# Kernel tuning notes

Hardware: AMD Instinct MI355X
Metric: run time of the kernel (lower is better)

The kernel has to match this reference:

```python
import jax, jax.numpy as jnp
import numpy as np


def setup_inputs() -> dict:
    key = jax.random.key(0)
    k1, k2, k3, k4, k5, k6 = jax.random.split(key, 6)
    B, N, D, H = 32, 4096, 256, 256
    return {
        "queries": jax.random.normal(k1, (B, N, D), dtype=jnp.float32),
        "keys": jax.random.normal(k2, (B, N, D), dtype=jnp.float32),
        "values": jax.random.normal(k3, (B, N, D), dtype=jnp.float32),
        "Wq": jax.random.normal(k4, (H, D), dtype=jnp.float32) * (1.0 / np.sqrt(D)),
        "Wk": jax.random.normal(k5, (H, D), dtype=jnp.float32) * (1.0 / np.sqrt(D)),
        "Wv": jax.random.normal(k6, (1, H), dtype=jnp.float32) * (1.0 / np.sqrt(H)),
    }


def reference(queries, keys, values, Wq, Wk, Wv):
    # Project queries and keys to hidden dim (torch Linear weight is [out, in])
    q = jnp.einsum('bnd,hd->bnh', queries, Wq)   # [B, N, H]
    k = jnp.einsum('bnd,hd->bnh', keys, Wk)      # [B, N, H]
    features = jnp.tanh(q + k)                   # [B, N, H]
    scores = jnp.einsum('bnh,oh->bno', features, Wv)  # [B, N, 1]
    alpha = jax.nn.softmax(scores, axis=1)       # softmax over N
    # dropout p=0 -> identity
    aggr_max = jnp.argmax(alpha, axis=1)         # [B, 1]
    out = jnp.sum(alpha * values, axis=1)        # [B, D]
    return (out, aggr_max)
```

## Files before the change

kernel.cpp:

```cpp
#include <hip/hip_runtime.h>

#define Bb 32
#define Nn 4096
#define Dd 256
#define Hh 256
#define NCH 32
#define CHUNK 128

typedef __attribute__((ext_vector_type(8))) _Float16 half8;
typedef __attribute__((ext_vector_type(4))) float f32x4;

#define GLDS16(gp, lp) __builtin_amdgcn_global_load_lds( \
    (const __attribute__((address_space(1))) unsigned int*)(gp), \
    (__attribute__((address_space(3))) unsigned int*)(lp), 16, 0, 0)

__device__ __forceinline__ float fast_tanhf(float x) {
    float e = __expf(2.0f * x);
    return 1.0f - 2.0f / (e + 1.0f);
}

__device__ __forceinline__ half8 cvt8(f32x4 v0, f32x4 v1) {
    half8 h;
    h[0] = (_Float16)v0.x; h[1] = (_Float16)v0.y;
    h[2] = (_Float16)v0.z; h[3] = (_Float16)v0.w;
    h[4] = (_Float16)v1.x; h[5] = (_Float16)v1.y;
    h[6] = (_Float16)v1.z; h[7] = (_Float16)v1.w;
    return h;
}

__global__ __launch_bounds__(256) void prep_w_kernel(
    const float* __restrict__ Wq, const float* __restrict__ Wk,
    _Float16* __restrict__ Wf)
{
    const int g = blockIdx.x * 256 + threadIdx.x;
    const int s = g >> 10;
    const int j = (g >> 6) & 15;
    const int l = g & 63;
    const int n = j * 16 + (l & 15);
    const int k = s * 32 + (l >> 4) * 8;
    const float* src = (k < 256) ? (Wq + n * 256 + k) : (Wk + n * 256 + (k - 256));
    const f32x4 v0 = *(const f32x4*)src;
    const f32x4 v1 = *(const f32x4*)(src + 4);
    *(half8*)&Wf[(size_t)g * 8] = cvt8(v0, v1);
}

__global__ __launch_bounds__(256, 3) void scores_dma_kernel(
    const float* __restrict__ Q, const float* __restrict__ Kmat,
    const _Float16* __restrict__ Wf,
    const float* __restrict__ Wv, float* __restrict__ scores)
{
    __shared__ float Abuf[2][4096];
    __shared__ float red[4][64];

    const int tid = threadIdx.x;
    const int lane = tid & 63;
    const int wave = tid >> 6;
    const size_t row0 = (size_t)blockIdx.x * 64;

    f32x4 acc[4][4];
#pragma unroll
    for (int m = 0; m < 4; ++m)
#pragma unroll
        for (int n = 0; n < 4; ++n) acc[m][n] = (f32x4){0.f, 0.f, 0.f, 0.f};

    float wv[4];
#pragma unroll
    for (int n = 0; n < 4; ++n) wv[n] = Wv[wave * 64 + n * 16 + (lane & 15)];

    int eoff[4];
#pragma unroll
    for (int j = 0; j < 4; ++j) {
        const int i = wave * 4 + j;
        const int kk = i >> 3;
        const int m  = (i >> 1) & 3;
        const int row_local = m * 16 + ((lane >> 1) & 15);
        const int kloc = kk * 32 + ((i & 1) * 2 + (lane >> 5)) * 8 + (lane & 1) * 4;
        eoff[j] = row_local * Dd + kloc;
    }

    half8 BB[8];
    auto issue_b = [&](int s) {
#pragma unroll
        for (int kk = 0; kk < 2; ++kk)
#pragma unroll
            for (int n = 0; n < 4; ++n)
                BB[kk * 4 + n] = *(const half8*)(Wf +
                    ((size_t)((s * 2 + kk) * 16 + wave * 4 + n) * 64 + lane) * 8);
    };
    auto dma_a = [&](int buf, int s) {
        const float* base = (s < 4) ? (Q    + row0 * Dd + s * 64)
                                    : (Kmat + row0 * Dd + (s - 4) * 64);
        char* lbase = (char*)&Abuf[buf][0] + wave * 4096;
#pragma unroll
        for (int j = 0; j < 4; ++j)
            GLDS16(base + eoff[j], lbase + j * 1024);
    };
    auto cluster = [&](int buf) {
        __builtin_amdgcn_s_setprio(1);
#pragma unroll
        for (int kk = 0; kk < 2; ++kk)
#pragma unroll
            for (int m = 0; m < 4; ++m) {
                const float* fp = &Abuf[buf][(kk * 256 + m * 64 + lane) * 8];
                const f32x4 lo = *(const f32x4*)fp;
                const f32x4 hi = *(const f32x4*)(fp + 4);
                const half8 a = cvt8(lo, hi);
#pragma unroll
                for (int n = 0; n < 4; ++n)
                    acc[m][n] = __builtin_amdgcn_mfma_f32_16x16x32_f16(a, BB[kk * 4 + n], acc[m][n], 0, 0, 0);
            }
        __builtin_amdgcn_s_setprio(0);
    };

    dma_a(0, 0);
    __syncthreads();

    for (int s = 0; s < 8; ++s) {
        issue_b(s);
        if (s < 7) dma_a((s + 1) & 1, s + 1);
        cluster(s & 1);
        __syncthreads();
    }

    const int q = lane >> 4;
    float rp[4][4];
#pragma unroll
    for (int m = 0; m < 4; ++m)
#pragma unroll
        for (int r = 0; r < 4; ++r) {
            float v = 0.f;
#pragma unroll
            for (int n = 0; n < 4; ++n)
                v += wv[n] * fast_tanhf(acc[m][n][r]);
            rp[m][r] = v;
        }
#pragma unroll
    for (int mask = 1; mask <= 8; mask <<= 1)
#pragma unroll
        for (int m = 0; m < 4; ++m)
#pragma unroll
            for (int r = 0; r < 4; ++r)
                rp[m][r] += __shfl_xor(rp[m][r], mask, 64);

    if ((lane & 15) == 0) {
#pragma unroll
        for (int m = 0; m < 4; ++m)
#pragma unroll
            for (int r = 0; r < 4; ++r)
                red[wave][m * 16 + q * 4 + r] = rp[m][r];
    }
    __syncthreads();
    if (tid < 64)
        scores[row0 + tid] = (red[0][tid] + red[1][tid]) + (red[2][tid] + red[3][tid]);
}

#define MAXC 64
__global__ __launch_bounds__(256) void softmax_reduce_kernel(
    const float* __restrict__ scores,
    const float* __restrict__ Qg, const float* __restrict__ Kg,
    const float* __restrict__ Wq, const float* __restrict__ Wk,
    const float* __restrict__ Wv,
    float* __restrict__ mbuf, float* __restrict__ zbuf, float* __restrict__ out)
{
    __shared__ float sv[256];
    __shared__ int si[256];
    __shared__ double dred[256];
    __shared__ int cand[MAXC];
    __shared__ int cnt;
    const int b = blockIdx.x;
    const int tid = threadIdx.x;
    const float* sc = scores + (size_t)b * Nn;

    float best = -1e30f; int bi = 0;
    for (int j = 0; j < Nn / 256; ++j) {
        const int n = tid + j * 256;
        const float v = sc[n];
        if (v > best) { best = v; bi = n; }
    }
    sv[tid] = best; si[tid] = bi;
    __syncthreads();
    for (int off = 128; off > 0; off >>= 1) {
        if (tid < off) {
            const float v2 = sv[tid + off]; const int i2 = si[tid + off];
            if (v2 > sv[tid] || (v2 == sv[tid] && i2 < si[tid])) { sv[tid] = v2; si[tid] = i2; }
        }
        __syncthreads();
    }
    const float m = sv[0];
    int amax = si[0];
    __syncthreads();

    float ssum = 0.f;
    for (int j = 0; j < Nn / 256; ++j) ssum += __expf(sc[tid + j * 256] - m);
    sv[tid] = ssum;
    __syncthreads();
    for (int off = 128; off > 0; off >>= 1) {
        if (tid < off) sv[tid] += sv[tid + off];
        __syncthreads();
    }
    const float Z = sv[0];
    __syncthreads();

    if (tid == 0) cnt = 0;
    __syncthreads();
    const float tau = 0.02f;
    for (int j = 0; j < Nn / 256; ++j) {
        const int n = tid + j * 256;
        if (sc[n] >= m - tau) {
            const int p = atomicAdd(&cnt, 1);
            if (p < MAXC) cand[p] = n;
        }
    }
    __syncthreads();
    const int ncand = (cnt < MAXC) ? cnt : MAXC;
    if (ncand > 1) {
        double bestv = -1e300; int besti = 0x7fffffff;
        for (int c = 0; c < ncand; ++c) {
            const int n = cand[c];
            const float* qr = Qg + ((size_t)b * Nn + n) * Dd;
            const float* kr = Kg + ((size_t)b * Nn + n) * Dd;
            const float* wqr = Wq + tid * Dd;
            const float* wkr = Wk + tid * Dd;
            double accd = 0.0;
            for (int k2 = 0; k2 < Dd; ++k2)
                accd += (double)qr[k2] * (double)wqr[k2] + (double)kr[k2] * (double)wkr[k2];
            dred[tid] = (double)Wv[tid] * tanh(accd);
            __syncthreads();
            for (int off = 128; off > 0; off >>= 1) {
                if (tid < off) dred[tid] += dred[tid + off];
                __syncthreads();
            }
            const double s_c = dred[0];
            __syncthreads();
            if (s_c > bestv || (s_c == bestv && n < besti)) { bestv = s_c; besti = n; }
        }
        amax = besti;
    }

    if (tid == 0) {
        mbuf[b] = m;
        zbuf[b] = Z;
        out[(size_t)Bb * Dd + b] = (float)amax;
    }
}

__global__ __launch_bounds__(256) void partial_kernel(
    const float* __restrict__ V, const float* __restrict__ scores,
    const float* __restrict__ mbuf, float* __restrict__ part)
{
    __shared__ float e[CHUNK];
    const int c = blockIdx.x;
    const int b = blockIdx.y;
    const int tid = threadIdx.x;
    const float m = mbuf[b];
    if (tid < CHUNK)
        e[tid] = __expf(scores[(size_t)b * Nn + (size_t)c * CHUNK + tid] - m);
    __syncthreads();

    const float* vp = V + ((size_t)b * Nn + (size_t)c * CHUNK) * Dd + tid;
    float a0 = 0.f, a1 = 0.f, a2 = 0.f, a3 = 0.f;
    for (int n = 0; n < CHUNK; n += 4) {
        a0 = fmaf(e[n + 0], vp[(size_t)(n + 0) * Dd], a0);
        a1 = fmaf(e[n + 1], vp[(size_t)(n + 1) * Dd], a1);
        a2 = fmaf(e[n + 2], vp[(size_t)(n + 2) * Dd], a2);
        a3 = fmaf(e[n + 3], vp[(size_t)(n + 3) * Dd], a3);
    }
    part[((size_t)b * NCH + c) * Dd + tid] = ((a0 + a1) + (a2 + a3));
}

__global__ __launch_bounds__(256) void finalize_kernel(
    const float* __restrict__ part, const float* __restrict__ zbuf,
    float* __restrict__ out)
{
    const int b = blockIdx.x;
    const int tid = threadIdx.x;
    float s = 0.f;
#pragma unroll
    for (int c = 0; c < NCH; ++c) s += part[((size_t)b * NCH + c) * Dd + tid];
    out[(size_t)b * Dd + tid] = s / zbuf[b];
}

extern "C" void kernel_launch(void* const* d_in, const int* in_sizes, int n_in,
                              void* d_out, int out_size, void* d_ws, size_t ws_size,
                              hipStream_t stream) {
    const float* Q  = (const float*)d_in[0];
    const float* K  = (const float*)d_in[1];
    const float* V  = (const float*)d_in[2];
    const float* Wq = (const float*)d_in[3];
    const float* Wk = (const float*)d_in[4];
    const float* Wv = (const float*)d_in[5];
    float* out = (float*)d_out;

    char* wsb = (char*)d_ws;
    _Float16* Wf  = (_Float16*)(wsb);
    float* scores = (float*)(wsb + 262144);
    float* mbuf   = (float*)(wsb + 786432);
    float* zbuf   = (float*)(wsb + 786432 + 128);
    float* part   = (float*)(wsb + 786432 + 256);

    prep_w_kernel<<<dim3(64), dim3(256), 0, stream>>>(Wq, Wk, Wf);
    scores_dma_kernel<<<dim3((Bb * Nn) / 64), dim3(256), 0, stream>>>(Q, K, Wf, Wv, scores);
    softmax_reduce_kernel<<<dim3(Bb), dim3(256), 0, stream>>>(scores, Q, K, Wq, Wk, Wv, mbuf, zbuf, out);
    partial_kernel<<<dim3(NCH, Bb), dim3(256), 0, stream>>>(V, scores, mbuf, part);
    finalize_kernel<<<dim3(Bb), dim3(256), 0, stream>>>(part, zbuf, out);
}
```

Measured before the change: 146.3 us.

## Load full A tile once as fp16 into LDS instead of double-buffered DMA

Replaces the double-buffered global_load_lds pipeline over 8 K-stages with a single up-front load of each block's whole 64x512 Q|K tile. The tile is converted to fp16 in registers before being written to LDS, so the MFMA loop reads half8 directly with no per-stage conversion and no per-stage __syncthreads. B-fragment loads are ping-ponged between two register sets. In exchange there is no overlap between the global loads and compute within a block, and occupancy hints drop from 3 to 2 blocks per CU because LDS use grows to 64KB.

```diff
diff --git a/kernel.cpp b/kernel.cpp
--- a/kernel.cpp
+++ b/kernel.cpp
@@ -9,10 +9,6 @@
 
 typedef __attribute__((ext_vector_type(8))) _Float16 half8;
 typedef __attribute__((ext_vector_type(4))) float f32x4;
-
-#define GLDS16(gp, lp) __builtin_amdgcn_global_load_lds( \
-    (const __attribute__((address_space(1))) unsigned int*)(gp), \
-    (__attribute__((address_space(3))) unsigned int*)(lp), 16, 0, 0)
 
 __device__ __forceinline__ float fast_tanhf(float x) {
     float e = __expf(2.0f * x);
@@ -44,12 +40,12 @@
     *(half8*)&Wf[(size_t)g * 8] = cvt8(v0, v1);
 }
 
-__global__ __launch_bounds__(256, 3) void scores_dma_kernel(
+__global__ __launch_bounds__(256, 2) void scores_oneshot_kernel(
     const float* __restrict__ Q, const float* __restrict__ Kmat,
     const _Float16* __restrict__ Wf,
     const float* __restrict__ Wv, float* __restrict__ scores)
 {
-    __shared__ float Abuf[2][4096];
+    __shared__ _Float16 Af[64 * 512];
     __shared__ float red[4][64];
 
     const int tid = threadIdx.x;
@@ -67,60 +63,58 @@
 #pragma unroll
     for (int n = 0; n < 4; ++n) wv[n] = Wv[wave * 64 + n * 16 + (lane & 15)];
 
-    int eoff[4];
-#pragma unroll
-    for (int j = 0; j < 4; ++j) {
-        const int i = wave * 4 + j;
-        const int kk = i >> 3;
-        const int m  = (i >> 1) & 3;
-        const int row_local = m * 16 + ((lane >> 1) & 15);
-        const int kloc = kk * 32 + ((i & 1) * 2 + (lane >> 5)) * 8 + (lane & 1) * 4;
-        eoff[j] = row_local * Dd + kloc;
-    }
-
-    half8 BB[8];
-    auto issue_b = [&](int s) {
-#pragma unroll
-        for (int kk = 0; kk < 2; ++kk)
+    half8 BA[4], BB[4];
+    auto loadB_A = [&](int gs) {
+#pragma unroll
+        for (int n = 0; n < 4; ++n)
+            BA[n] = *(const half8*)(Wf + ((size_t)(gs * 16 + wave * 4 + n) * 64 + lane) * 8);
+    };
+    auto loadB_B = [&](int gs) {
+#pragma unroll
+        for (int n = 0; n < 4; ++n)
+            BB[n] = *(const half8*)(Wf + ((size_t)(gs * 16 + wave * 4 + n) * 64 + lane) * 8);
+    };
+
+    loadB_A(0);
+    {
+        const float* src = (wave < 2)
+            ? (Q    + (row0 + lane) * Dd + wave * 128)
+            : (Kmat + (row0 + lane) * Dd + (wave - 2) * 128);
+        const int m = lane >> 4;
+        const int rl = lane & 15;
+#pragma unroll
+        for (int g = 0; g < 16; ++g) {
+            const f32x4 v0 = *(const f32x4*)(src + g * 8);
+            const f32x4 v1 = *(const f32x4*)(src + g * 8 + 4);
+            const int gs = wave * 4 + (g >> 2);
+            const int sub = g & 3;
+            *(half8*)&Af[((gs * 4 + m) * 64 + sub * 16 + rl) * 8] = cvt8(v0, v1);
+        }
+    }
+    __syncthreads();
+
+    __builtin_amdgcn_s_setprio(1);
+#pragma unroll
+    for (int g2 = 0; g2 < 8; ++g2) {
+        const int gs = 2 * g2;
+        loadB_B(gs + 1);
+#pragma unroll
+        for (int m = 0; m < 4; ++m) {
+            const half8 a = *(const half8*)&Af[((gs * 4 + m) * 64 + lane) * 8];
 #pragma unroll
             for (int n = 0; n < 4; ++n)
-                BB[kk * 4 + n] = *(const half8*)(Wf +
-                    ((size_t)((s * 2 + kk) * 16 + wave * 4 + n) * 64 + lane) * 8);
-    };
-    auto dma_a = [&](int buf, int s) {
-        const float* base = (s < 4) ? (Q    + row0 * Dd + s * 64)
-                                    : (Kmat + row0 * Dd + (s - 4) * 64);
-        char* lbase = (char*)&Abuf[buf][0] + wave * 4096;
-#pragma unroll
-        for (int j = 0; j < 4; ++j)
-            GLDS16(base + eoff[j], lbase + j * 1024);
-    };
-    auto cluster = [&](int buf) {
-        __builtin_amdgcn_s_setprio(1);
-#pragma unroll
-        for (int kk = 0; kk < 2; ++kk)
-#pragma unroll
-            for (int m = 0; m < 4; ++m) {
-                const float* fp = &Abuf[buf][(kk * 256 + m * 64 + lane) * 8];
-                const f32x4 lo = *(const f32x4*)fp;
-                const f32x4 hi = *(const f32x4*)(fp + 4);
-                const half8 a = cvt8(lo, hi);
-#pragma unroll
-                for (int n = 0; n < 4; ++n)
-                    acc[m][n] = __builtin_amdgcn_mfma_f32_16x16x32_f16(a, BB[kk * 4 + n], acc[m][n], 0, 0, 0);
-            }
-        __builtin_amdgcn_s_setprio(0);
-    };
-
-    dma_a(0, 0);
-    __syncthreads();
-
-    for (int s = 0; s < 8; ++s) {
-        issue_b(s);
-        if (s < 7) dma_a((s + 1) & 1, s + 1);
-        cluster(s & 1);
-        __syncthreads();
-    }
+                acc[m][n] = __builtin_amdgcn_mfma_f32_16x16x32_f16(a, BA[n], acc[m][n], 0, 0, 0);
+        }
+        if (gs + 2 < 16) loadB_A(gs + 2);
+#pragma unroll
+        for (int m = 0; m < 4; ++m) {
+            const half8 a = *(const half8*)&Af[(((gs + 1) * 4 + m) * 64 + lane) * 8];
+#pragma unroll
+            for (int n = 0; n < 4; ++n)
+                acc[m][n] = __builtin_amdgcn_mfma_f32_16x16x32_f16(a, BB[n], acc[m][n], 0, 0, 0);
+        }
+    }
+    __builtin_amdgcn_s_setprio(0);
 
     const int q = lane >> 4;
     float rp[4][4];
@@ -299,7 +293,7 @@
     float* part   = (float*)(wsb + 786432 + 256);
 
     prep_w_kernel<<<dim3(64), dim3(256), 0, stream>>>(Wq, Wk, Wf);
-    scores_dma_kernel<<<dim3((Bb * Nn) / 64), dim3(256), 0, stream>>>(Q, K, Wf, Wv, scores);
+    scores_oneshot_kernel<<<dim3((Bb * Nn) / 64), dim3(256), 0, stream>>>(Q, K, Wf, Wv, scores);
     softmax_reduce_kernel<<<dim3(Bb), dim3(256), 0, stream>>>(scores, Q, K, Wq, Wk, Wv, mbuf, zbuf, out);
     partial_kernel<<<dim3(NCH, Bb), dim3(256), 0, stream>>>(V, scores, mbuf, part);
     finalize_kernel<<<dim3(Bb), dim3(256), 0, stream>>>(part, zbuf, out);
```

Measured after the change: 159.4 us. +8.9%, slower.

## Split scores kernel into producer and consumer waves with fp16 LDS triple buffer

Applied to the files above, without the earlier changes.

Replaces the global_load_lds DMA path with warp specialization. Two extra producer waves load Q/K fp32 rows into registers, convert them to fp16 and write them into a triple-buffered LDS tile in MFMA fragment order. Four consumer waves now only read ready half8 fragments and run MFMAs, so the conversion work moves off the MFMA critical path and LDS traffic is halved. The cost is 384-thread blocks, higher register pressure from the prefetch registers, and fewer lanes issuing global loads.

```diff
diff --git a/kernel.cpp b/kernel.cpp
--- a/kernel.cpp
+++ b/kernel.cpp
@@ -6,13 +6,10 @@
 #define Hh 256
 #define NCH 32
 #define CHUNK 128
+#define NSTEP 8
 
 typedef __attribute__((ext_vector_type(8))) _Float16 half8;
 typedef __attribute__((ext_vector_type(4))) float f32x4;
-
-#define GLDS16(gp, lp) __builtin_amdgcn_global_load_lds( \
-    (const __attribute__((address_space(1))) unsigned int*)(gp), \
-    (__attribute__((address_space(3))) unsigned int*)(lp), 16, 0, 0)
 
 __device__ __forceinline__ float fast_tanhf(float x) {
     float e = __expf(2.0f * x);
@@ -44,12 +41,12 @@
     *(half8*)&Wf[(size_t)g * 8] = cvt8(v0, v1);
 }
 
-__global__ __launch_bounds__(256, 3) void scores_dma_kernel(
-    const float* __restrict__ Q, const float* __restrict__ Kmat,
+__global__ __launch_bounds__(384, 3) void scores_pc_kernel(
+    const float* __restrict__ Qm, const float* __restrict__ Km,
     const _Float16* __restrict__ Wf,
     const float* __restrict__ Wv, float* __restrict__ scores)
 {
-    __shared__ float Abuf[2][4096];
+    __shared__ _Float16 Af[3][4096];
     __shared__ float red[4][64];
 
     const int tid = threadIdx.x;
@@ -62,92 +59,132 @@
     for (int m = 0; m < 4; ++m)
 #pragma unroll
         for (int n = 0; n < 4; ++n) acc[m][n] = (f32x4){0.f, 0.f, 0.f, 0.f};
-
     float wv[4];
-#pragma unroll
-    for (int n = 0; n < 4; ++n) wv[n] = Wv[wave * 64 + n * 16 + (lane & 15)];
-
-    int eoff[4];
-#pragma unroll
-    for (int j = 0; j < 4; ++j) {
-        const int i = wave * 4 + j;
-        const int kk = i >> 3;
-        const int m  = (i >> 1) & 3;
-        const int row_local = m * 16 + ((lane >> 1) & 15);
-        const int kloc = kk * 32 + ((i & 1) * 2 + (lane >> 5)) * 8 + (lane & 1) * 4;
-        eoff[j] = row_local * Dd + kloc;
-    }
-
-    half8 BB[8];
-    auto issue_b = [&](int s) {
+    half8 BA[8], BB[8];
+
+    f32x4 Pa[8], Pb[8];
+    int roff[4], slot[4];
+
+    if (wave < 4) {
+#pragma unroll
+        for (int n = 0; n < 4; ++n) wv[n] = Wv[wave * 64 + n * 16 + (lane & 15)];
+    } else {
+#pragma unroll
+        for (int j = 0; j < 4; ++j) {
+            const int lin = j * 128 + (wave - 4) * 64 + lane;
+            const int r = lin >> 3;
+            const int c8 = lin & 7;
+            roff[j] = r * Dd + c8 * 8;
+            const int kk = c8 >> 2, sub = c8 & 3, m = r >> 4, fl = (r & 15) + sub * 16;
+            slot[j] = ((kk * 4 + m) * 64 + fl) * 8;
+        }
+    }
+
+    auto loadB = [&](int s, half8* B) {
 #pragma unroll
         for (int kk = 0; kk < 2; ++kk)
 #pragma unroll
             for (int n = 0; n < 4; ++n)
-                BB[kk * 4 + n] = *(const half8*)(Wf +
-                    ((size_t)((s * 2 + kk) * 16 + wave * 4 + n) * 64 + lane) * 8);
-    };
-    auto dma_a = [&](int buf, int s) {
-        const float* base = (s < 4) ? (Q    + row0 * Dd + s * 64)
-                                    : (Kmat + row0 * Dd + (s - 4) * 64);
-        char* lbase = (char*)&Abuf[buf][0] + wave * 4096;
+                B[kk * 4 + n] = *(const half8*)(Wf +
+                    ((size_t)((2 * s + kk) * 16 + wave * 4 + n) * 64 + lane) * 8);
+    };
+    auto issueP = [&](int s) {
+        const float* base = (s < 4) ? (Qm + row0 * Dd + s * 64)
+                                    : (Km + row0 * Dd + (s - 4) * 64);
+#pragma unroll
+        for (int j = 0; j < 4; ++j) {
+            Pa[2 * j]     = *(const f32x4*)(base + roff[j]);
+            Pa[2 * j + 1] = *(const f32x4*)(base + roff[j] + 4);
+        }
+    };
+    auto issueQ = [&](int s) {
+        const float* base = (s < 4) ? (Qm + row0 * Dd + s * 64)
+                                    : (Km + row0 * Dd + (s - 4) * 64);
+#pragma unroll
+        for (int j = 0; j < 4; ++j) {
+            Pb[2 * j]     = *(const f32x4*)(base + roff[j]);
+            Pb[2 * j + 1] = *(const f32x4*)(base + roff[j] + 4);
+        }
+    };
+    auto writeP = [&](int buf) {
 #pragma unroll
         for (int j = 0; j < 4; ++j)
-            GLDS16(base + eoff[j], lbase + j * 1024);
-    };
-    auto cluster = [&](int buf) {
-        __builtin_amdgcn_s_setprio(1);
+            *(half8*)&Af[buf][slot[j]] = cvt8(Pa[2 * j], Pa[2 * j + 1]);
+    };
+    auto writeQ = [&](int buf) {
+#pragma unroll
+        for (int j = 0; j < 4; ++j)
+            *(half8*)&Af[buf][slot[j]] = cvt8(Pb[2 * j], Pb[2 * j + 1]);
+    };
+    auto mfma_step = [&](int buf, half8* B) {
 #pragma unroll
         for (int kk = 0; kk < 2; ++kk)
 #pragma unroll
             for (int m = 0; m < 4; ++m) {
-                const float* fp = &Abuf[buf][(kk * 256 + m * 64 + lane) * 8];
-                const f32x4 lo = *(const f32x4*)fp;
-                const f32x4 hi = *(const f32x4*)(fp + 4);
-                const half8 a = cvt8(lo, hi);
+                const half8 a = *(const half8*)&Af[buf][((kk * 4 + m) * 64 + lane) * 8];
 #pragma unroll
                 for (int n = 0; n < 4; ++n)
-                    acc[m][n] = __builtin_amdgcn_mfma_f32_16x16x32_f16(a, BB[kk * 4 + n], acc[m][n], 0, 0, 0);
+                    acc[m][n] = __builtin_amdgcn_mfma_f32_16x16x32_f16(a, B[kk * 4 + n], acc[m][n], 0, 0, 0);
             }
-        __builtin_amdgcn_s_setprio(0);
-    };
-
-    dma_a(0, 0);
-    __syncthreads();
-
-    for (int s = 0; s < 8; ++s) {
-        issue_b(s);
-        if (s < 7) dma_a((s + 1) & 1, s + 1);
-        cluster(s & 1);
+    };
+
+    if (wave < 4) {
+        loadB(0, BA);
+    } else {
+        issueP(0);
+        issueQ(1);
+        writeP(0);
+    }
+    __syncthreads();
+
+#pragma unroll
+    for (int s2 = 0; s2 < 4; ++s2) {
+        const int s = 2 * s2;
+        if (wave < 4) {
+            if (s + 1 < NSTEP) loadB(s + 1, BB);
+            mfma_step(s % 3, BA);
+        } else {
+            if (s + 2 < NSTEP) issueP(s + 2);
+            if (s + 1 < NSTEP) writeQ((s + 1) % 3);
+        }
         __syncthreads();
-    }
-
-    const int q = lane >> 4;
-    float rp[4][4];
-#pragma unroll
-    for (int m = 0; m < 4; ++m)
-#pragma unroll
-        for (int r = 0; r < 4; ++r) {
-            float v = 0.f;
-#pragma unroll
-            for (int n = 0; n < 4; ++n)
-                v += wv[n] * fast_tanhf(acc[m][n][r]);
-            rp[m][r] = v;
-        }
-#pragma unroll
-    for (int mask = 1; mask <= 8; mask <<= 1)
+        if (wave < 4) {
+            if (s + 2 < NSTEP) loadB(s + 2, BA);
+            mfma_step((s + 1) % 3, BB);
+        } else {
+            if (s + 3 < NSTEP) issueQ(s + 3);
+            if (s + 2 < NSTEP) writeP((s + 2) % 3);
+        }
+        __syncthreads();
+    }
+
+    if (wave < 4) {
+        const int q = lane >> 4;
+        float rp[4][4];
 #pragma unroll
         for (int m = 0; m < 4; ++m)
 #pragma unroll
-            for (int r = 0; r < 4; ++r)
-                rp[m][r] += __shfl_xor(rp[m][r], mask, 64);
-
-    if ((lane & 15) == 0) {
-#pragma unroll
-        for (int m = 0; m < 4; ++m)
-#pragma unroll
-            for (int r = 0; r < 4; ++r)
-                red[wave][m * 16 + q * 4 + r] = rp[m][r];
+            for (int r = 0; r < 4; ++r) {
+                float v = 0.f;
+#pragma unroll
+                for (int n = 0; n < 4; ++n)
+                    v += wv[n] * fast_tanhf(acc[m][n][r]);
+                rp[m][r] = v;
+            }
+#pragma unroll
+        for (int mask = 1; mask <= 8; mask <<= 1)
+#pragma unroll
+            for (int m = 0; m < 4; ++m)
+#pragma unroll
+                for (int r = 0; r < 4; ++r)
+                    rp[m][r] += __shfl_xor(rp[m][r], mask, 64);
+        if ((lane & 15) == 0) {
+#pragma unroll
+            for (int m = 0; m < 4; ++m)
+#pragma unroll
+                for (int r = 0; r < 4; ++r)
+                    red[wave][m * 16 + q * 4 + r] = rp[m][r];
+        }
     }
     __syncthreads();
     if (tid < 64)
@@ -299,7 +336,7 @@
     float* part   = (float*)(wsb + 786432 + 256);
 
     prep_w_kernel<<<dim3(64), dim3(256), 0, stream>>>(Wq, Wk, Wf);
-    scores_dma_kernel<<<dim3((Bb * Nn) / 64), dim3(256), 0, stream>>>(Q, K, Wf, Wv, scores);
+    scores_pc_kernel<<<dim3((Bb * Nn) / 64), dim3(384), 0, stream>>>(Q, K, Wf, Wv, scores);
     softmax_reduce_kernel<<<dim3(Bb), dim3(256), 0, stream>>>(scores, Q, K, Wq, Wk, Wv, mbuf, zbuf, out);
     partial_kernel<<<dim3(NCH, Bb), dim3(256), 0, stream>>>(V, scores, mbuf, part);
     finalize_kernel<<<dim3(Bb), dim3(256), 0, stream>>>(part, zbuf, out);
```

Result: slower. 338.9 us (+131.7%).
